# Kernel tuning notes

Measured on AMD Instinct MI355X. Metric: run time of the kernel, lower is better.

## Reference

```python
import jax, jax.numpy as jnp
import numpy as np

EMBED_DIM = 1024
N_HEADS = 16
HEAD_DIM = EMBED_DIM // N_HEADS  # 64
ROPE_DIM = 4
N_FREQ = HEAD_DIM // (2 * ROPE_DIM)  # 8 rotary freqs per coordinate axis
ROPE_THETA = 10000.0
FFN_DIM = 4 * EMBED_DIM
N_TOK = 4096
N_SEQ = 8
EPS = 1e-5
NEG_INF = -1e30


def setup_inputs() -> dict:
    key = jax.random.key(0)
    ks = jax.random.split(key, 16)
    s = 0.02
    coords = jax.random.uniform(ks[0], (N_TOK, ROPE_DIM), jnp.float32) * 10.0
    feats = jax.random.normal(ks[1], (N_TOK, EMBED_DIM), jnp.float32)
    interior = jnp.sort(jax.random.randint(ks[2], (N_SEQ - 1,), 1, N_TOK)).astype(jnp.int32)
    cu_seqlens = jnp.concatenate([jnp.zeros((1,), jnp.int32), interior,
                                  jnp.full((1,), N_TOK, jnp.int32)])
    # learnable RoPE inverse frequencies, one bank per coordinate axis
    base = 1.0 / (ROPE_THETA ** (jnp.arange(N_FREQ, dtype=jnp.float32) * 2.0 * ROPE_DIM / HEAD_DIM))
    inv_freq = jnp.tile(base[None, :], (ROPE_DIM, 1))  # [rope_dim, n_freq]
    return {
        "coords": coords,
        "feats": feats,
        "cu_seqlens": cu_seqlens,
        "Wqkv": jax.random.normal(ks[3], (EMBED_DIM, 3 * EMBED_DIM), jnp.float32) * s,
        "bqkv": jnp.zeros((3 * EMBED_DIM,), jnp.float32),
        "Wo": jax.random.normal(ks[4], (EMBED_DIM, EMBED_DIM), jnp.float32) * s,
        "bo": jnp.zeros((EMBED_DIM,), jnp.float32),
        "inv_freq": inv_freq,
        "ln1_g": jnp.ones((EMBED_DIM,), jnp.float32),
        "ln1_b": jnp.zeros((EMBED_DIM,), jnp.float32),
        "W1": jax.random.normal(ks[5], (EMBED_DIM, FFN_DIM), jnp.float32) * s,
        "b1": jnp.zeros((FFN_DIM,), jnp.float32),
        "W2": jax.random.normal(ks[6], (FFN_DIM, EMBED_DIM), jnp.float32) * s,
        "b2": jnp.zeros((EMBED_DIM,), jnp.float32),
        "ln2_g": jnp.ones((EMBED_DIM,), jnp.float32),
        "ln2_b": jnp.zeros((EMBED_DIM,), jnp.float32),
    }


def _layernorm(x, g, b):
    mu = jnp.mean(x, axis=-1, keepdims=True)
    xc = x - mu
    var = jnp.mean(xc * xc, axis=-1, keepdims=True)
    return xc * jax.lax.rsqrt(var + EPS) * g + b


def _block_forward(coords, feats, cu_seqlens, Wqkv, bqkv, Wo, bo, inv_freq,
                   ln1_g, ln1_b, W1, b1, W2, b2, ln2_g, ln2_b):
    N, D = feats.shape
    qkv = (feats @ Wqkv + bqkv).reshape(N, 3, N_HEADS, HEAD_DIM)
    q, k, v = qkv[:, 0], qkv[:, 1], qkv[:, 2]  # each [N, H, hd]

    # multi-dimensional learnable RoPE: each coord axis rotates its freq bank
    ang = jnp.einsum('nd,df->ndf', coords, inv_freq).reshape(N, 1, HEAD_DIM // 2)
    cos, sin = jnp.cos(ang), jnp.sin(ang)

    def rot(x):
        x1, x2 = jnp.split(x, 2, axis=-1)
        return jnp.concatenate([x1 * cos - x2 * sin, x2 * cos + x1 * sin], axis=-1)

    q, k = rot(q), rot(k)

    # varlen block-diagonal attention mask from cu_seqlens
    seg = jnp.searchsorted(cu_seqlens[1:], jnp.arange(N), side='right')
    mask = seg[:, None] == seg[None, :]  # [N, N]

    scores = jnp.einsum('nhd,mhd->hnm', q, k) / np.sqrt(HEAD_DIM).astype(np.float32)
    scores = jnp.where(mask[None, :, :], scores, NEG_INF)
    attn = jax.nn.softmax(scores, axis=-1)
    o = jnp.einsum('hnm,mhd->nhd', attn, v).reshape(N, D) @ Wo + bo

    h = _layernorm(feats + o, ln1_g, ln1_b)
    f = jax.nn.gelu(h @ W1 + b1) @ W2 + b2
    return _layernorm(h + f, ln2_g, ln2_b)


def reference(coords, feats, cu_seqlens, Wqkv, bqkv, Wo, bo, inv_freq,
              ln1_g, ln1_b, W1, b1, W2, b2, ln2_g, ln2_b):
    return _block_forward(coords, feats, cu_seqlens, Wqkv, bqkv, Wo, bo, inv_freq,
                          ln1_g, ln1_b, W1, b1, W2, b2, ln2_g, ln2_b)
```

## Files before the change

kernel.cpp:

```cpp
#include <hip/hip_runtime.h>

#define NTOK 4096
#define EMB  1024
#define NH   16
#define HD   64
#define FFN  4096

typedef __bf16 bf16x8 __attribute__((ext_vector_type(8)));
typedef float  f32x4  __attribute__((ext_vector_type(4)));

#define ASG __attribute__((address_space(1)))
#define ASL __attribute__((address_space(3)))

__device__ __forceinline__ float b2f(unsigned short u) {
    union { unsigned int i; float f; } v; v.i = ((unsigned int)u) << 16; return v.f;
}
__device__ __forceinline__ unsigned short f2b(float f) {
    return __builtin_bit_cast(unsigned short, (__bf16)f);
}
__device__ __forceinline__ float ldf(const void* p, size_t i, int f32) {
    return f32 ? ((const float*)p)[i] : b2f(((const unsigned short*)p)[i]);
}
__device__ __forceinline__ int probe_f32(const void* p) {
    return ((const unsigned int*)p)[0] == 0x3F800000u ? 1 : 0;
}
__device__ __forceinline__ float gelu_f(float x) {
    float z = 0.7978845608028654f * (x + 0.044715f * x * x * x);
    float t = 1.0f - 2.0f / (__expf(2.0f * z) + 1.0f);
    return 0.5f * x * (1.0f + t);
}
__device__ __forceinline__ void gll16(const void* g, void* l) {
    __builtin_amdgcn_global_load_lds((const ASG void*)g, (ASL void*)l, 16, 0, 0);
}

__global__ __launch_bounds__(256) void convert_kernel(
    const void* __restrict__ feats, const void* __restrict__ bqkv,
    const void* __restrict__ bo, const void* __restrict__ b1,
    const void* __restrict__ b2, const void* __restrict__ g1,
    const void* __restrict__ e1, const void* __restrict__ g2,
    const void* __restrict__ e2, const int* __restrict__ cu,
    unsigned short* __restrict__ feats_bf, unsigned short* __restrict__ smalls,
    int* __restrict__ seg, const void* __restrict__ pr) {
    const int f32 = probe_f32(pr);
    int bid = blockIdx.x, tid = threadIdx.x;
    if (bid < 4096) {
        size_t base = (size_t)bid * 1024 + tid * 4;
        union { unsigned short u[4]; int2 v; } U;
#pragma unroll
        for (int i = 0; i < 4; ++i) U.u[i] = f2b(ldf(feats, base + i, f32));
        *reinterpret_cast<int2*>(&feats_bf[base]) = U.v;
    } else if (bid < 4109) {
        int flat = (bid - 4096) * 1024 + tid * 4;
        const void* src; int off;
        if      (flat < 3072)  { src = bqkv; off = 0; }
        else if (flat < 4096)  { src = bo;   off = 3072; }
        else if (flat < 8192)  { src = b1;   off = 4096; }
        else if (flat < 9216)  { src = b2;   off = 8192; }
        else if (flat < 10240) { src = g1;   off = 9216; }
        else if (flat < 11264) { src = e1;   off = 10240; }
        else if (flat < 12288) { src = g2;   off = 11264; }
        else                   { src = e2;   off = 12288; }
        union { unsigned short u[4]; int2 v; } U;
#pragma unroll
        for (int i = 0; i < 4; ++i) U.u[i] = f2b(ldf(src, flat - off + i, f32));
        *reinterpret_cast<int2*>(&smalls[flat]) = U.v;
    } else {
        int n = (bid - 4109) * 256 + tid;
        int s = 0;
#pragma unroll
        for (int i = 1; i <= 8; ++i) s += (cu[i] <= n) ? 1 : 0;
        seg[n] = s;
    }
}

__global__ __launch_bounds__(64) void sched_kernel(
    const int* __restrict__ seg, const int* __restrict__ cu,
    int* __restrict__ perm) {
    __shared__ int w[64];
    int t = threadIdx.x;
    int s0 = seg[t * 64], s1 = seg[t * 64 + 63];
    int kb = cu[s0] & ~63;
    int kend = cu[s1 + 1];
    w[t] = (kend - kb + 63) >> 6;
    __syncthreads();
    int wt = w[t], r = 0;
#pragma unroll
    for (int j = 0; j < 64; ++j) {
        int wj = w[j];
        r += (wj > wt || (wj == wt && j < t)) ? 1 : 0;
    }
    perm[r] = t;
}

__global__ __launch_bounds__(256) void transpose_kernel(
    const void* __restrict__ W, unsigned short* __restrict__ O,
    int K, int N, const void* __restrict__ pr) {
    const int f32 = probe_f32(pr);
    int b = blockIdx.x, tid = threadIdx.x;
    int ntiles = N >> 6;
    int nt = b % ntiles, kt = b / ntiles;
    __shared__ unsigned short T[64][66];
    int cx = (tid & 15) * 4, ry = tid >> 4;
#pragma unroll
    for (int i = 0; i < 4; ++i) {
        int k = kt * 64 + ry + 16 * i;
        size_t base = (size_t)k * N + nt * 64 + cx;
#pragma unroll
        for (int j = 0; j < 4; ++j)
            T[ry + 16 * i][cx + j] = f2b(ldf(W, base + j, f32));
    }
    __syncthreads();
#pragma unroll
    for (int i = 0; i < 4; ++i) {
        int n = nt * 64 + ry + 16 * i;
        union { unsigned short u[4]; int2 v; } U;
#pragma unroll
        for (int j = 0; j < 4; ++j) U.u[j] = T[cx + j][ry + 16 * i];
        *reinterpret_cast<int2*>(&O[(size_t)n * K + kt * 64 + cx]) = U.v;
    }
}

template <int ACT, int OUTEXT, int TN, int SPLITV, int SPLITK>
__global__ __launch_bounds__(256) void gemm128(
    const unsigned short* __restrict__ A, const unsigned short* __restrict__ Bt,
    const unsigned short* __restrict__ bias, void* __restrict__ C,
    void* __restrict__ C2,
    int M, int N, int K, int lda, int ldb, const void* __restrict__ pr) {
    constexpr int NB = TN / 32;
    __shared__ __align__(16) unsigned short As[128 * 64];
    __shared__ __align__(16) unsigned short Bs[TN * 64];
    const int f32 = OUTEXT ? probe_f32(pr) : 0;
    const int tid = threadIdx.x;
    const int wave = tid >> 6, lane = tid & 63;
    const int wy = wave >> 1, wx = wave & 1;
    const int qm = lane & 15, quad = lane >> 4;
    const int z = SPLITK ? (int)blockIdx.z : 0;
    int bx, by;
    if ((gridDim.y & 7) == 0) {
        int lin = blockIdx.y * gridDim.x + blockIdx.x;
        int ypg = gridDim.y >> 3;
        int xcd = lin & 7, s = lin >> 3;
        int sy = s / gridDim.x;
        by = xcd * ypg + sy;
        bx = s - sy * gridDim.x;
    } else { bx = blockIdx.x; by = blockIdx.y; }
    const int m0 = by * 128, n0 = bx * TN;
    const int r = lane >> 3, gl = lane & 7;

    f32x4 acc[4][NB];
#pragma unroll
    for (int i = 0; i < 4; ++i)
#pragma unroll
        for (int j = 0; j < NB; ++j) acc[i][j] = (f32x4){0.f, 0.f, 0.f, 0.f};

    const int koff = SPLITK ? z * K : 0;
    const unsigned short* Ab = A  + (size_t)m0 * lda + koff;
    const unsigned short* Bb = Bt + (size_t)n0 * ldb + koff;

    for (int k0 = 0; k0 < K; k0 += 64) {
#pragma unroll
        for (int i = 0; i < 4; ++i) {
            int cc = wave * 4 + i;
            gll16(Ab + (size_t)(8 * cc + r) * lda + k0 + ((gl ^ r) << 3), &As[cc * 512]);
        }
#pragma unroll
        for (int i = 0; i < NB; ++i) {
            int cc = wave * NB + i;
            gll16(Bb + (size_t)(8 * cc + r) * ldb + k0 + ((gl ^ r) << 3), &Bs[cc * 512]);
        }
        __syncthreads();
#pragma unroll
        for (int h = 0; h < 2; ++h) {
            bf16x8 af[4], bfr[NB];
#pragma unroll
            for (int i = 0; i < 4; ++i) {
                int phys = (((h * 4 + quad) ^ (qm & 7)) << 3);
                af[i] = *reinterpret_cast<const bf16x8*>(&As[(64 * wy + 16 * i + qm) * 64 + phys]);
            }
#pragma unroll
            for (int j = 0; j < NB; ++j) {
                int phys = (((h * 4 + quad) ^ (qm & 7)) << 3);
                bfr[j] = *reinterpret_cast<const bf16x8*>(&Bs[((TN / 2) * wx + 16 * j + qm) * 64 + phys]);
            }
#pragma unroll
            for (int i = 0; i < 4; ++i)
#pragma unroll
                for (int j = 0; j < NB; ++j)
                    acc[i][j] = __builtin_amdgcn_mfma_f32_16x16x32_bf16(af[i], bfr[j], acc[i][j], 0, 0, 0);
        }
        __syncthreads();
    }
#pragma unroll
    for (int j = 0; j < NB; ++j) {
        int col = n0 + (TN / 2) * wx + 16 * j + qm;
        float bv = (SPLITK && z) ? 0.f : b2f(bias[col]);
        if (SPLITV && n0 >= 2048) {
            int d = col - 2048;
#pragma unroll
            for (int i = 0; i < 4; ++i) {
                int rowb = m0 + 64 * wy + 16 * i + quad * 4;
                union { unsigned short u[4]; int2 v; } U;
#pragma unroll
                for (int rr = 0; rr < 4; ++rr) U.u[rr] = f2b(acc[i][j][rr] + bv);
                *reinterpret_cast<int2*>((unsigned short*)C2 + (size_t)d * 4096 + rowb) = U.v;
            }
        } else {
            const int ldc = SPLITV ? 2048 : N;
            void* Cz = (SPLITK && z) ? C2 : C;
#pragma unroll
            for (int i = 0; i < 4; ++i) {
                int rowb = m0 + 64 * wy + 16 * i + quad * 4;
#pragma unroll
                for (int rr = 0; rr < 4; ++rr) {
                    size_t idx = (size_t)(rowb + rr) * ldc + col;
                    float v = acc[i][j][rr] + bv;
                    if (ACT == 1) v = gelu_f(v);
                    if (OUTEXT && f32) ((float*)Cz)[idx] = v;
                    else               ((unsigned short*)Cz)[idx] = f2b(v);
                }
            }
        }
    }
}

__global__ __launch_bounds__(512, 2) void gemm256_ffn1(
    const unsigned short* __restrict__ A, const unsigned short* __restrict__ Bt,
    const unsigned short* __restrict__ bias, unsigned short* __restrict__ C) {
    __shared__ __align__(16) unsigned short L[2][2][256][64];
    const int tid = threadIdx.x;
    const int wv = tid >> 6, lane = tid & 63;
    const int wm = wv >> 2, wn = wv & 3;
    const int qm = lane & 15, quad = lane >> 4;
    const int r8 = lane >> 3, gl = lane & 7;
    const int xsw = (gl ^ r8) << 3;
    int lin = blockIdx.y * 16 + blockIdx.x;
    int xcd = lin & 7, s = lin >> 3;
    int by = xcd * 2 + (s >> 4), bx = s & 15;
    const int m0 = by * 256, n0 = bx * 256;
    const unsigned short* Ab = A  + (size_t)m0 * 1024;
    const unsigned short* Bb = Bt + (size_t)n0 * 1024;

    f32x4 acc[8][4];
#pragma unroll
    for (int i = 0; i < 8; ++i)
#pragma unroll
        for (int j = 0; j < 4; ++j) acc[i][j] = (f32x4){0.f, 0.f, 0.f, 0.f};
    bf16x8 af[4], bf[4];

#define STG(buf, ten, sl, kn)                                                      \
    gll16(((ten) ? Bb : Ab) + (size_t)(64 * (sl) + 8 * wv + r8) * 1024 + (kn) + xsw, \
          &L[buf][ten][64 * (sl) + 8 * wv][0])
#define RD(mh, h)                                                                  \
    {                                                                              \
        const int phys = ((((h) * 4) + quad) ^ (qm & 7)) << 3;                     \
        _Pragma("unroll")                                                          \
        for (int i = 0; i < 4; ++i)                                                \
            af[i] = *reinterpret_cast<const bf16x8*>(                              \
                &Ac[(wm * 128 + (mh) * 64 + i * 16 + qm) * 64 + phys]);            \
        _Pragma("unroll")                                                          \
        for (int j = 0; j < 4; ++j)                                                \
            bf[j] = *reinterpret_cast<const bf16x8*>(                              \
                &Bc[(wn * 64 + j * 16 + qm) * 64 + phys]);                         \
    }
#define MM(mh, h)                                                                  \
    _Pragma("unroll")                                                              \
    for (int i = 0; i < 4; ++i)                                                    \
        _Pragma("unroll")                                                          \
        for (int j = 0; j < 4; ++j)                                                \
            acc[(mh) * 4 + i][j] = __builtin_amdgcn_mfma_f32_16x16x32_bf16(        \
                af[i], bf[j], acc[(mh) * 4 + i][j], 0, 0, 0);

    STG(0, 0, 0, 0); STG(0, 0, 2, 0);
    STG(0, 1, 0, 0); STG(0, 1, 1, 0); STG(0, 1, 2, 0); STG(0, 1, 3, 0);
    STG(0, 0, 1, 0); STG(0, 0, 3, 0);
    asm volatile("s_waitcnt vmcnt(2)" ::: "memory");
    __builtin_amdgcn_s_barrier();

    for (int t = 0; t < 16; ++t) {
        const unsigned short* Ac = &L[t & 1][0][0][0];
        const unsigned short* Bc = &L[t & 1][1][0][0];
        const int nb = (t + 1) & 1;
        const int kn = (t + 1) << 6;
        const bool more = t < 15;
        RD(0, 0);
        if (more) { STG(nb, 0, 0, kn); STG(nb, 0, 2, kn); }
        __builtin_amdgcn_s_barrier();
        asm volatile("s_waitcnt lgkmcnt(0)" ::: "memory");
        __builtin_amdgcn_s_setprio(1); MM(0, 0); __builtin_amdgcn_s_setprio(0);
        __builtin_amdgcn_s_barrier();
        RD(0, 1);
        if (more) {
            STG(nb, 1, 0, kn); STG(nb, 1, 1, kn);
            asm volatile("s_waitcnt vmcnt(4)" ::: "memory");
        } else {
            asm volatile("s_waitcnt vmcnt(0)" ::: "memory");
        }
        __builtin_amdgcn_s_barrier();
        asm volatile("s_waitcnt lgkmcnt(0)" ::: "memory");
        __builtin_amdgcn_s_setprio(1); MM(0, 1); __builtin_amdgcn_s_setprio(0);
        __builtin_amdgcn_s_barrier();
        RD(1, 0);
        if (more) { STG(nb, 1, 2, kn); STG(nb, 1, 3, kn); }
        __builtin_amdgcn_s_barrier();
        asm volatile("s_waitcnt lgkmcnt(0)" ::: "memory");
        __builtin_amdgcn_s_setprio(1); MM(1, 0); __builtin_amdgcn_s_setprio(0);
        __builtin_amdgcn_s_barrier();
        RD(1, 1);
        if (more) {
            STG(nb, 0, 1, kn); STG(nb, 0, 3, kn);
            asm volatile("s_waitcnt vmcnt(2)" ::: "memory");
        }
        __builtin_amdgcn_s_barrier();
        asm volatile("s_waitcnt lgkmcnt(0)" ::: "memory");
        __builtin_amdgcn_s_setprio(1); MM(1, 1); __builtin_amdgcn_s_setprio(0);
        __builtin_amdgcn_s_barrier();
    }
#undef STG
#undef RD
#undef MM
#pragma unroll
    for (int j = 0; j < 4; ++j) {
        int col = n0 + wn * 64 + j * 16 + qm;
        float bv = b2f(bias[col]);
#pragma unroll
        for (int i = 0; i < 8; ++i) {
            int rowb = m0 + wm * 128 + i * 16 + quad * 4;
#pragma unroll
            for (int rr = 0; rr < 4; ++rr) {
                float v = gelu_f(acc[i][j][rr] + bv);
                C[(size_t)(rowb + rr) * 4096 + col] = f2b(v);
            }
        }
    }
}

__global__ __launch_bounds__(256) void rope_kernel(
    const void* __restrict__ coords, const void* __restrict__ inv_freq,
    unsigned short* __restrict__ qk, const void* __restrict__ pr) {
    const int f32 = probe_f32(pr);
    int n = blockIdx.x, tid = threadIdx.x;
#pragma unroll
    for (int it = 0; it < 2; ++it) {
        int idx = tid + it * 256;
        int hh = idx >> 5, f = idx & 31;
        float c  = ldf(coords, n * 4 + (f >> 3), f32);
        float iv = ldf(inv_freq, f, f32);
        float sn, cs;
        sincosf(c * iv, &sn, &cs);
#pragma unroll
        for (int w = 0; w < 2; ++w) {
            size_t base = (size_t)n * 2048 + (size_t)w * 1024 + hh * 64;
            float scl = w ? 1.0f : 0.125f;
            float x1 = b2f(qk[base + f]);
            float x2 = b2f(qk[base + 32 + f]);
            qk[base + f]      = f2b((x1 * cs - x2 * sn) * scl);
            qk[base + 32 + f] = f2b((x2 * cs + x1 * sn) * scl);
        }
    }
}

__global__ __launch_bounds__(256) void attn_part(
    const unsigned short* __restrict__ qk, const unsigned short* __restrict__ vt,
    const int* __restrict__ seg, const int* __restrict__ cu,
    const int* __restrict__ perm,
    unsigned short* __restrict__ u0, unsigned short* __restrict__ u1,
    unsigned short* __restrict__ u2, float* __restrict__ ml) {
    const int h = blockIdx.x / 3;
    const int piece = blockIdx.x - 3 * h;
    const int t3 = perm[blockIdx.y];
    const int t0 = t3 * 64;
    const int tid  = threadIdx.x;
    const int wave = tid >> 6, lane = tid & 63;
    const int qm = lane & 15, quad = lane >> 4;

    __shared__ __align__(16) unsigned short Ks[2][64][64];
    __shared__ __align__(16) unsigned short Vs[2][80][64];
    __shared__ __align__(16) unsigned short Ps[64][64];
    __shared__ int segq[64], segk[2][64];

    const unsigned short* qrow = qk + (size_t)(t0 + 16 * wave + qm) * 2048 + h * 64;
    bf16x8 af0 = *reinterpret_cast<const bf16x8*>(qrow + quad * 8);
    bf16x8 af1 = *reinterpret_cast<const bf16x8*>(qrow + 32 + quad * 8);

    {
        int rr = tid >> 4, cc = (tid & 15) * 4;
        unsigned short val = (rr == 0) ? (unsigned short)0x3F80 : (unsigned short)0;
#pragma unroll
        for (int b = 0; b < 2; ++b)
#pragma unroll
            for (int j = 0; j < 4; ++j) Vs[b][64 + rr][cc + j] = val;
    }
    if (tid < 64) segq[tid] = seg[t0 + tid];
    __syncthreads();

    const int kbegA = cu[segq[0]] & ~63;
    const int kendT = cu[segq[63] + 1];
    const int nchunks = (kendT - kbegA + 63) >> 6;
    const int third = (nchunks + 2) / 3;
    const int kb = kbegA + piece * third * 64;
    const int ke = min(kendT, kbegA + (piece + 1) * third * 64);

    int sqr[4];
#pragma unroll
    for (int r = 0; r < 4; ++r) sqr[r] = segq[16 * wave + quad * 4 + r];
    const int wsmin = segq[16 * wave];
    const int wsmax = segq[16 * wave + 15];

    float m[4];
    f32x4 o[5];
#pragma unroll
    for (int r = 0; r < 4; ++r) m[r] = -1e30f;
#pragma unroll
    for (int t = 0; t < 5; ++t) o[t] = (f32x4){0.f, 0.f, 0.f, 0.f};

    const int krow = tid >> 2, kdc = (tid & 3) * 16;
    const int k7 = krow & 7;
    const int sw0 = (((tid & 3) * 2) ^ k7) << 3;
    const int sw1 = ((((tid & 3) * 2 + 1)) ^ k7) << 3;
    const int rsw0 = (quad ^ (qm & 7)) << 3;
    const int rsw1 = ((quad + 4) ^ (qm & 7)) << 3;
    int4 kA, kB, vA, vB; int sg;
#define LOAD_CHUNK(KC)                                                                   \
    {                                                                                    \
        const unsigned short* kp = qk + (size_t)((KC) + krow) * 2048 + 1024 + h * 64 + kdc; \
        kA = *reinterpret_cast<const int4*>(kp);                                         \
        kB = *reinterpret_cast<const int4*>(kp + 8);                                     \
        const unsigned short* vp = vt + (size_t)(h * 64 + krow) * 4096 + (KC) + kdc;     \
        vA = *reinterpret_cast<const int4*>(vp);                                         \
        vB = *reinterpret_cast<const int4*>(vp + 8);                                     \
        sg = 127;                                                                        \
        if (tid < 64 && (KC) + tid < ke) sg = seg[(KC) + tid];                           \
    }
#define STORE_CHUNK(B)                                                                   \
    {                                                                                    \
        *reinterpret_cast<int4*>(&Ks[B][krow][sw0]) = kA;                                \
        *reinterpret_cast<int4*>(&Ks[B][krow][sw1]) = kB;                                \
        *reinterpret_cast<int4*>(&Vs[B][krow][sw0]) = vA;                                \
        *reinterpret_cast<int4*>(&Vs[B][krow][sw1]) = vB;                                \
        if (tid < 64) segk[B][tid] = sg;                                                 \
    }

    int cur = 0;
    if (kb < ke) {
        LOAD_CHUNK(kb);
        STORE_CHUNK(0);
    }

    for (int kc = kb; kc < ke; kc += 64) {
        const bool have_next = (kc + 64 < ke);
        if (have_next) LOAD_CHUNK(kc + 64);
        __syncthreads();

        const int skmin = segk[cur][0], skmax = segk[cur][63];
        const bool act = !(skmax < wsmin || skmin > wsmax);

        if (act) {
            f32x4 sc[4];
#pragma unroll
            for (int nb = 0; nb < 4; ++nb) {
                bf16x8 bf0 = *reinterpret_cast<const bf16x8*>(&Ks[cur][16 * nb + qm][rsw0]);
                bf16x8 bf1 = *reinterpret_cast<const bf16x8*>(&Ks[cur][16 * nb + qm][rsw1]);
                f32x4 s = (f32x4){0.f, 0.f, 0.f, 0.f};
                s = __builtin_amdgcn_mfma_f32_16x16x32_bf16(af0, bf0, s, 0, 0, 0);
                s = __builtin_amdgcn_mfma_f32_16x16x32_bf16(af1, bf1, s, 0, 0, 0);
                sc[nb] = s;
            }
            if (!((skmin == skmax) & (wsmin == wsmax))) {
#pragma unroll
                for (int nb = 0; nb < 4; ++nb) {
                    int sk = segk[cur][16 * nb + qm];
#pragma unroll
                    for (int r = 0; r < 4; ++r)
                        sc[nb][r] = (sk == sqr[r]) ? sc[nb][r] : -1e30f;
                }
            }
            float alpha[4];
#pragma unroll
            for (int r = 0; r < 4; ++r) {
                float v = fmaxf(fmaxf(sc[0][r], sc[1][r]), fmaxf(sc[2][r], sc[3][r]));
                v = fmaxf(v, __shfl_xor(v, 1, 64));
                v = fmaxf(v, __shfl_xor(v, 2, 64));
                v = fmaxf(v, __shfl_xor(v, 4, 64));
                v = fmaxf(v, __shfl_xor(v, 8, 64));
                float mn = fmaxf(m[r], v);
                alpha[r] = __expf(m[r] - mn);
                m[r] = mn;
            }
#pragma unroll
            for (int nb = 0; nb < 4; ++nb) {
#pragma unroll
                for (int r = 0; r < 4; ++r) {
                    float p = __expf(sc[nb][r] - m[r]);
                    int row = 16 * wave + quad * 4 + r;
                    int phys = (((2 * nb + (qm >> 3)) ^ ((quad * 4 + r) & 7)) << 3) + (qm & 7);
                    Ps[row][phys] = f2b(p);
                }
            }
#pragma unroll
            for (int t = 0; t < 5; ++t)
#pragma unroll
                for (int r = 0; r < 4; ++r) o[t][r] *= alpha[r];

            bf16x8 pa0 = *reinterpret_cast<const bf16x8*>(&Ps[16 * wave + qm][rsw0]);
            bf16x8 pa1 = *reinterpret_cast<const bf16x8*>(&Ps[16 * wave + qm][rsw1]);
#pragma unroll
            for (int dt = 0; dt < 4; ++dt) {
                bf16x8 vb0 = *reinterpret_cast<const bf16x8*>(&Vs[cur][16 * dt + qm][rsw0]);
                bf16x8 vb1 = *reinterpret_cast<const bf16x8*>(&Vs[cur][16 * dt + qm][rsw1]);
                o[dt] = __builtin_amdgcn_mfma_f32_16x16x32_bf16(pa0, vb0, o[dt], 0, 0, 0);
                o[dt] = __builtin_amdgcn_mfma_f32_16x16x32_bf16(pa1, vb1, o[dt], 0, 0, 0);
            }
            {
                bf16x8 vb0 = *reinterpret_cast<const bf16x8*>(&Vs[cur][64 + qm][rsw0]);
                bf16x8 vb1 = *reinterpret_cast<const bf16x8*>(&Vs[cur][64 + qm][rsw1]);
                o[4] = __builtin_amdgcn_mfma_f32_16x16x32_bf16(pa0, vb0, o[4], 0, 0, 0);
                o[4] = __builtin_amdgcn_mfma_f32_16x16x32_bf16(pa1, vb1, o[4], 0, 0, 0);
            }
        }
        if (have_next) {
            STORE_CHUNK(cur ^ 1);
        }
        cur ^= 1;
    }
#undef LOAD_CHUNK
#undef STORE_CHUNK
    unsigned short* dst = (piece == 0) ? u0 : ((piece == 1) ? u1 : u2);
#pragma unroll
    for (int dt = 0; dt < 4; ++dt)
#pragma unroll
        for (int r = 0; r < 4; ++r) {
            int row = t0 + 16 * wave + quad * 4 + r;
            dst[(size_t)row * 1024 + h * 64 + 16 * dt + qm] = f2b(o[dt][r]);
        }
    if (qm == 0) {
        float2* ML = (float2*)ml;
#pragma unroll
        for (int r = 0; r < 4; ++r) {
            int row = t0 + 16 * wave + quad * 4 + r;
            ML[((piece * 16 + h) << 12) + row] = make_float2(m[r], o[4][r]);
        }
    }
}

__global__ __launch_bounds__(256) void combine_kernel(
    const unsigned short* __restrict__ u1, const unsigned short* __restrict__ u2,
    const float* __restrict__ ml, unsigned short* __restrict__ u0out) {
    int n = blockIdx.x, tid = threadIdx.x;
    int d4 = tid * 4, h = tid >> 4;
    const float2* ML = (const float2*)ml;
    float2 p0 = ML[(h << 12) + n];
    float2 p1 = ML[((16 + h) << 12) + n];
    float2 p2 = ML[((32 + h) << 12) + n];
    float M = fmaxf(p0.x, fmaxf(p1.x, p2.x));
    float a0 = __expf(p0.x - M), a1 = __expf(p1.x - M), a2 = __expf(p2.x - M);
    float rcp = 1.0f / (a0 * p0.y + a1 * p1.y + a2 * p2.y);
    size_t ix = (size_t)n * 1024 + d4;
    union { int2 q; unsigned short u[4]; } A, B, Cq, R;
    A.q  = *reinterpret_cast<const int2*>(u0out + ix);
    B.q  = *reinterpret_cast<const int2*>(u1 + ix);
    Cq.q = *reinterpret_cast<const int2*>(u2 + ix);
#pragma unroll
    for (int i = 0; i < 4; ++i)
        R.u[i] = f2b((a0 * b2f(A.u[i]) + a1 * b2f(B.u[i]) + a2 * b2f(Cq.u[i])) * rcp);
    *reinterpret_cast<int2*>(u0out + ix) = R.q;
}

template <int OUTEXT>
__global__ __launch_bounds__(256) void ln3_kernel(
    const unsigned short* __restrict__ x1, const unsigned short* __restrict__ x2a,
    const unsigned short* __restrict__ x2b,
    const unsigned short* __restrict__ g, const unsigned short* __restrict__ b,
    void* __restrict__ out, const void* __restrict__ pr) {
    const int f32 = probe_f32(pr);
    int n = blockIdx.x, tid = threadIdx.x;
    __shared__ float red[8];
    const int d0 = tid * 4;
    const size_t ix0 = (size_t)n * EMB + d0;
    float v[4];
    {
        union { int2 q; unsigned short u[4]; } A, Ba, Bb2;
        A.q   = *reinterpret_cast<const int2*>(&x1[ix0]);
        Ba.q  = *reinterpret_cast<const int2*>(&x2a[ix0]);
        Bb2.q = *reinterpret_cast<const int2*>(&x2b[ix0]);
#pragma unroll
        for (int i = 0; i < 4; ++i)
            v[i] = b2f(A.u[i]) + b2f(Ba.u[i]) + b2f(Bb2.u[i]);
    }
    float s = v[0] + v[1] + v[2] + v[3];
#pragma unroll
    for (int off = 1; off < 64; off <<= 1) s += __shfl_xor(s, off, 64);
    if ((tid & 63) == 0) red[tid >> 6] = s;
    __syncthreads();
    float mu = (red[0] + red[1] + red[2] + red[3]) * (1.0f / 1024.0f);
    float sq = 0.0f;
#pragma unroll
    for (int i = 0; i < 4; ++i) { float c = v[i] - mu; sq += c * c; }
#pragma unroll
    for (int off = 1; off < 64; off <<= 1) sq += __shfl_xor(sq, off, 64);
    if ((tid & 63) == 0) red[4 + (tid >> 6)] = sq;
    __syncthreads();
    float var = (red[4] + red[5] + red[6] + red[7]) * (1.0f / 1024.0f);
    float rcp = rsqrtf(var + 1e-5f);
    union { int2 q; unsigned short u[4]; } G, Bb;
    G.q  = *reinterpret_cast<const int2*>(&g[d0]);
    Bb.q = *reinterpret_cast<const int2*>(&b[d0]);
    if (OUTEXT && f32) {
        float4 R;
        R.x = (v[0] - mu) * rcp * b2f(G.u[0]) + b2f(Bb.u[0]);
        R.y = (v[1] - mu) * rcp * b2f(G.u[1]) + b2f(Bb.u[1]);
        R.z = (v[2] - mu) * rcp * b2f(G.u[2]) + b2f(Bb.u[2]);
        R.w = (v[3] - mu) * rcp * b2f(G.u[3]) + b2f(Bb.u[3]);
        *reinterpret_cast<float4*>((float*)out + ix0) = R;
    } else {
        union { int2 q; unsigned short u[4]; } R;
#pragma unroll
        for (int i = 0; i < 4; ++i)
            R.u[i] = f2b((v[i] - mu) * rcp * b2f(G.u[i]) + b2f(Bb.u[i]));
        *reinterpret_cast<int2*>((unsigned short*)out + ix0) = R.q;
    }
}

extern "C" void kernel_launch(void* const* d_in, const int* in_sizes, int n_in,
                              void* d_out, int out_size, void* d_ws, size_t ws_size,
                              hipStream_t stream) {
    const void* coords   = d_in[0];
    const void* feats    = d_in[1];
    const int*  cu       = (const int*)d_in[2];
    const void* Wqkv     = d_in[3];
    const void* bqkv     = d_in[4];
    const void* Wo       = d_in[5];
    const void* bo       = d_in[6];
    const void* inv_freq = d_in[7];
    const void* ln1_g    = d_in[8];
    const void* ln1_b    = d_in[9];
    const void* W1       = d_in[10];
    const void* b1       = d_in[11];
    const void* W2       = d_in[12];
    const void* b2       = d_in[13];
    const void* ln2_g    = d_in[14];
    const void* ln2_b    = d_in[15];
    const void* pr = ln1_g;

    char* ws = (char*)d_ws;
    int* seg = (int*)ws;
    unsigned short* smalls   = (unsigned short*)(ws + 16384);
    unsigned short* bqkv_bf  = smalls;
    unsigned short* bo_bf    = smalls + 3072;
    unsigned short* b1_bf    = smalls + 4096;
    unsigned short* b2_bf    = smalls + 8192;
    unsigned short* g1_bf    = smalls + 9216;
    unsigned short* e1_bf    = smalls + 10240;
    unsigned short* g2_bf    = smalls + 11264;
    unsigned short* e2_bf    = smalls + 12288;
    int* perm                = (int*)(ws + 49152);
    unsigned short* feats_bf = (unsigned short*)(ws + 65536);
    unsigned short* hbuf     = feats_bf;
    unsigned short* W1_t     = (unsigned short*)(ws + 8454144);
    unsigned short* u1buf    = (unsigned short*)(ws + 16842752);
    unsigned short* Wqkv_t   = (unsigned short*)(ws + 18939904);
    unsigned short* qkbuf    = (unsigned short*)(ws + 25231360);
    unsigned short* vtbuf    = (unsigned short*)(ws + 42008576);
    unsigned short* attn_o   = (unsigned short*)(ws + 50397184);
    unsigned short* Wo_t     = (unsigned short*)(ws + 18939904);
    unsigned short* woP0     = (unsigned short*)(ws + 25231360);
    unsigned short* woP1     = (unsigned short*)(ws + 33619968);
    unsigned short* f1       = (unsigned short*)(ws + 25231360);
    unsigned short* ffP0     = (unsigned short*)(ws + 8454144);
    unsigned short* ffP1     = (unsigned short*)(ws + 16842752);
    float* mlbuf = (float*)d_out;
    unsigned short* u2buf = (unsigned short*)((char*)d_out + 2097152);
    unsigned short* W2_t  = (unsigned short*)((char*)d_out + 8388608);

    hipLaunchKernelGGL(convert_kernel, dim3(4125), dim3(256), 0, stream,
                       feats, bqkv, bo, b1, b2, ln1_g, ln1_b, ln2_g, ln2_b, cu,
                       feats_bf, smalls, seg, pr);
    hipLaunchKernelGGL(sched_kernel, dim3(1), dim3(64), 0, stream,
                       seg, cu, perm);
    hipLaunchKernelGGL(transpose_kernel, dim3(768), dim3(256), 0, stream,
                       Wqkv, Wqkv_t, 1024, 3072, pr);
    hipLaunchKernelGGL(transpose_kernel, dim3(1024), dim3(256), 0, stream,
                       W1, W1_t, 1024, 4096, pr);
    hipLaunchKernelGGL((gemm128<0, 0, 128, 1, 0>), dim3(24, 32), dim3(256), 0, stream,
                       feats_bf, Wqkv_t, bqkv_bf, qkbuf, vtbuf, NTOK, 3072, 1024, 1024, 1024, pr);
    hipLaunchKernelGGL(rope_kernel, dim3(NTOK), dim3(256), 0, stream,
                       coords, inv_freq, qkbuf, pr);
    hipLaunchKernelGGL(attn_part, dim3(48, 64), dim3(256), 0, stream,
                       qkbuf, vtbuf, seg, cu, perm, attn_o, u1buf, u2buf, mlbuf);
    hipLaunchKernelGGL(combine_kernel, dim3(NTOK), dim3(256), 0, stream,
                       u1buf, u2buf, mlbuf, attn_o);
    hipLaunchKernelGGL(transpose_kernel, dim3(256), dim3(256), 0, stream,
                       Wo, Wo_t, 1024, 1024, pr);
    hipLaunchKernelGGL((gemm128<0, 0, 128, 0, 1>), dim3(8, 32, 2), dim3(256), 0, stream,
                       attn_o, Wo_t, bo_bf, woP0, woP1, NTOK, 1024, 512, 1024, 1024, pr);
    hipLaunchKernelGGL(transpose_kernel, dim3(1024), dim3(256), 0, stream,
                       W2, W2_t, 4096, 1024, pr);
    hipLaunchKernelGGL((ln3_kernel<0>), dim3(NTOK), dim3(256), 0, stream,
                       feats_bf, woP0, woP1, g1_bf, e1_bf, hbuf, pr);
    hipLaunchKernelGGL(gemm256_ffn1, dim3(16, 16), dim3(512), 0, stream,
                       hbuf, W1_t, b1_bf, f1);
    hipLaunchKernelGGL((gemm128<0, 0, 128, 0, 1>), dim3(8, 32, 2), dim3(256), 0, stream,
                       f1, W2_t, b2_bf, ffP0, ffP1, NTOK, 1024, 2048, 4096, 4096, pr);
    hipLaunchKernelGGL((ln3_kernel<1>), dim3(NTOK), dim3(256), 0, stream,
                       hbuf, ffP0, ffP1, g2_bf, e2_bf, d_out, pr);
}
```

Before: 378.3 us.

## Fuse prep, schedule and weight transposes into one kernel; fold RoPE into QKV GEMM

Merges the conversion, scheduling and three weight-transpose launches into a single prep kernel, which cuts launch count and lets independent small jobs share one grid. RoPE rotation and Q scaling move into the QKV GEMM epilogue, so qkbuf is no longer written, reread and rewritten by a separate pass. Wo_t is moved into a buffer in d_out so it does not clash with qkbuf. The epilogue writes scalar bf16 values per lane with strided addresses and recomputes sincos for every element, so store efficiency may be lower than the old packed path.

```diff
diff --git a/kernel.cpp b/kernel.cpp
--- a/kernel.cpp
+++ b/kernel.cpp
@@ -33,14 +33,45 @@
     __builtin_amdgcn_global_load_lds((const ASG void*)g, (ASL void*)l, 16, 0, 0);
 }
 
-__global__ __launch_bounds__(256) void convert_kernel(
+__device__ __forceinline__ void transpose_body(
+    const void* __restrict__ W, unsigned short* __restrict__ O,
+    int K, int N, int b, int f32, unsigned short (*T)[66], int tid) {
+    int ntiles = N >> 6;
+    int nt = b % ntiles, kt = b / ntiles;
+    int cx = (tid & 15) * 4, ry = tid >> 4;
+#pragma unroll
+    for (int i = 0; i < 4; ++i) {
+        int k = kt * 64 + ry + 16 * i;
+        size_t base = (size_t)k * N + nt * 64 + cx;
+#pragma unroll
+        for (int j = 0; j < 4; ++j)
+            T[ry + 16 * i][cx + j] = f2b(ldf(W, base + j, f32));
+    }
+    __syncthreads();
+#pragma unroll
+    for (int i = 0; i < 4; ++i) {
+        int n = nt * 64 + ry + 16 * i;
+        union { unsigned short u[4]; int2 v; } U;
+#pragma unroll
+        for (int j = 0; j < 4; ++j) U.u[j] = T[cx + j][ry + 16 * i];
+        *reinterpret_cast<int2*>(&O[(size_t)n * K + kt * 64 + cx]) = U.v;
+    }
+}
+
+__global__ __launch_bounds__(256) void prep_kernel(
     const void* __restrict__ feats, const void* __restrict__ bqkv,
     const void* __restrict__ bo, const void* __restrict__ b1,
     const void* __restrict__ b2, const void* __restrict__ g1,
     const void* __restrict__ e1, const void* __restrict__ g2,
     const void* __restrict__ e2, const int* __restrict__ cu,
+    const void* __restrict__ Wqkv, const void* __restrict__ W1,
+    const void* __restrict__ Wo,
     unsigned short* __restrict__ feats_bf, unsigned short* __restrict__ smalls,
-    int* __restrict__ seg, const void* __restrict__ pr) {
+    int* __restrict__ seg, int* __restrict__ perm,
+    unsigned short* __restrict__ Wqkv_t, unsigned short* __restrict__ W1_t,
+    unsigned short* __restrict__ Wo_t, const void* __restrict__ pr) {
+    __shared__ unsigned short T[64][66];
+    __shared__ int w[64];
     const int f32 = probe_f32(pr);
     int bid = blockIdx.x, tid = threadIdx.x;
     if (bid < 4096) {
@@ -64,72 +95,63 @@
 #pragma unroll
         for (int i = 0; i < 4; ++i) U.u[i] = f2b(ldf(src, flat - off + i, f32));
         *reinterpret_cast<int2*>(&smalls[flat]) = U.v;
-    } else {
+    } else if (bid < 4125) {
         int n = (bid - 4109) * 256 + tid;
         int s = 0;
 #pragma unroll
         for (int i = 1; i <= 8; ++i) s += (cu[i] <= n) ? 1 : 0;
         seg[n] = s;
-    }
-}
-
-__global__ __launch_bounds__(64) void sched_kernel(
-    const int* __restrict__ seg, const int* __restrict__ cu,
-    int* __restrict__ perm) {
-    __shared__ int w[64];
-    int t = threadIdx.x;
-    int s0 = seg[t * 64], s1 = seg[t * 64 + 63];
-    int kb = cu[s0] & ~63;
-    int kend = cu[s1 + 1];
-    w[t] = (kend - kb + 63) >> 6;
-    __syncthreads();
-    int wt = w[t], r = 0;
-#pragma unroll
-    for (int j = 0; j < 64; ++j) {
-        int wj = w[j];
-        r += (wj > wt || (wj == wt && j < t)) ? 1 : 0;
-    }
-    perm[r] = t;
+    } else if (bid == 4125) {
+        if (tid < 64) {
+            int n0s = tid * 64, n1s = tid * 64 + 63;
+            int s0 = 0, s1 = 0;
+#pragma unroll
+            for (int i = 1; i <= 8; ++i) {
+                s0 += (cu[i] <= n0s) ? 1 : 0;
+                s1 += (cu[i] <= n1s) ? 1 : 0;
+            }
+            int kb = cu[s0] & ~63;
+            int kend = cu[s1 + 1];
+            w[tid] = (kend - kb + 63) >> 6;
+        }
+        __syncthreads();
+        if (tid < 64) {
+            int wt = w[tid], r = 0;
+#pragma unroll
+            for (int j = 0; j < 64; ++j) {
+                int wj = w[j];
+                r += (wj > wt || (wj == wt && j < tid)) ? 1 : 0;
+            }
+            perm[r] = tid;
+        }
+    } else if (bid < 4894) {
+        transpose_body(Wqkv, Wqkv_t, 1024, 3072, bid - 4126, f32, T, tid);
+    } else if (bid < 5918) {
+        transpose_body(W1, W1_t, 1024, 4096, bid - 4894, f32, T, tid);
+    } else {
+        transpose_body(Wo, Wo_t, 1024, 1024, bid - 5918, f32, T, tid);
+    }
 }
 
 __global__ __launch_bounds__(256) void transpose_kernel(
     const void* __restrict__ W, unsigned short* __restrict__ O,
     int K, int N, const void* __restrict__ pr) {
+    __shared__ unsigned short T[64][66];
     const int f32 = probe_f32(pr);
-    int b = blockIdx.x, tid = threadIdx.x;
-    int ntiles = N >> 6;
-    int nt = b % ntiles, kt = b / ntiles;
-    __shared__ unsigned short T[64][66];
-    int cx = (tid & 15) * 4, ry = tid >> 4;
-#pragma unroll
-    for (int i = 0; i < 4; ++i) {
-        int k = kt * 64 + ry + 16 * i;
-        size_t base = (size_t)k * N + nt * 64 + cx;
-#pragma unroll
-        for (int j = 0; j < 4; ++j)
-            T[ry + 16 * i][cx + j] = f2b(ldf(W, base + j, f32));
-    }
-    __syncthreads();
-#pragma unroll
-    for (int i = 0; i < 4; ++i) {
-        int n = nt * 64 + ry + 16 * i;
-        union { unsigned short u[4]; int2 v; } U;
-#pragma unroll
-        for (int j = 0; j < 4; ++j) U.u[j] = T[cx + j][ry + 16 * i];
-        *reinterpret_cast<int2*>(&O[(size_t)n * K + kt * 64 + cx]) = U.v;
-    }
-}
-
-template <int ACT, int OUTEXT, int TN, int SPLITV, int SPLITK>
+    transpose_body(W, O, K, N, blockIdx.x, f32, T, threadIdx.x);
+}
+
+template <int ACT, int OUTEXT, int TN, int SPLITV, int SPLITK, int ROPE>
 __global__ __launch_bounds__(256) void gemm128(
     const unsigned short* __restrict__ A, const unsigned short* __restrict__ Bt,
     const unsigned short* __restrict__ bias, void* __restrict__ C,
     void* __restrict__ C2,
-    int M, int N, int K, int lda, int ldb, const void* __restrict__ pr) {
+    int M, int N, int K, int lda, int ldb, const void* __restrict__ pr,
+    const void* __restrict__ coords, const void* __restrict__ inv_freq) {
     constexpr int NB = TN / 32;
     __shared__ __align__(16) unsigned short As[128 * 64];
     __shared__ __align__(16) unsigned short Bs[TN * 64];
-    const int f32 = OUTEXT ? probe_f32(pr) : 0;
+    const int f32 = (OUTEXT || ROPE) ? probe_f32(pr) : 0;
     const int tid = threadIdx.x;
     const int wave = tid >> 6, lane = tid & 63;
     const int wy = wave >> 1, wx = wave & 1;
@@ -189,6 +211,34 @@
                     acc[i][j] = __builtin_amdgcn_mfma_f32_16x16x32_bf16(af[i], bfr[j], acc[i][j], 0, 0, 0);
         }
         __syncthreads();
+    }
+    if (ROPE && n0 < 2048) {
+#pragma unroll
+        for (int jp = 0; jp < 2; ++jp) {
+            int colA = n0 + 64 * wx + 16 * jp + qm;
+            int colB = colA + 32;
+            int f = colA & 31;
+            float iv  = ldf(inv_freq, f, f32);
+            float bvA = b2f(bias[colA]);
+            float bvB = b2f(bias[colB]);
+            float scl = (colA < 1024) ? 0.125f : 1.0f;
+#pragma unroll
+            for (int i = 0; i < 4; ++i) {
+                int rowb = m0 + 64 * wy + 16 * i + quad * 4;
+#pragma unroll
+                for (int rr = 0; rr < 4; ++rr) {
+                    int row = rowb + rr;
+                    float c = ldf(coords, (size_t)row * 4 + (f >> 3), f32);
+                    float sn, cs;
+                    sincosf(c * iv, &sn, &cs);
+                    float x1 = acc[i][jp][rr] + bvA;
+                    float x2 = acc[i][jp + 2][rr] + bvB;
+                    ((unsigned short*)C)[(size_t)row * 2048 + colA] = f2b((x1 * cs - x2 * sn) * scl);
+                    ((unsigned short*)C)[(size_t)row * 2048 + colB] = f2b((x2 * cs + x1 * sn) * scl);
+                }
+            }
+        }
+        return;
     }
 #pragma unroll
     for (int j = 0; j < NB; ++j) {
@@ -330,31 +380,6 @@
                 float v = gelu_f(acc[i][j][rr] + bv);
                 C[(size_t)(rowb + rr) * 4096 + col] = f2b(v);
             }
-        }
-    }
-}
-
-__global__ __launch_bounds__(256) void rope_kernel(
-    const void* __restrict__ coords, const void* __restrict__ inv_freq,
-    unsigned short* __restrict__ qk, const void* __restrict__ pr) {
-    const int f32 = probe_f32(pr);
-    int n = blockIdx.x, tid = threadIdx.x;
-#pragma unroll
-    for (int it = 0; it < 2; ++it) {
-        int idx = tid + it * 256;
-        int hh = idx >> 5, f = idx & 31;
-        float c  = ldf(coords, n * 4 + (f >> 3), f32);
-        float iv = ldf(inv_freq, f, f32);
-        float sn, cs;
-        sincosf(c * iv, &sn, &cs);
-#pragma unroll
-        for (int w = 0; w < 2; ++w) {
-            size_t base = (size_t)n * 2048 + (size_t)w * 1024 + hh * 64;
-            float scl = w ? 1.0f : 0.125f;
-            float x1 = b2f(qk[base + f]);
-            float x2 = b2f(qk[base + 32 + f]);
-            qk[base + f]      = f2b((x1 * cs - x2 * sn) * scl);
-            qk[base + 32 + f] = f2b((x2 * cs + x1 * sn) * scl);
         }
     }
 }
@@ -661,7 +686,6 @@
     unsigned short* qkbuf    = (unsigned short*)(ws + 25231360);
     unsigned short* vtbuf    = (unsigned short*)(ws + 42008576);
     unsigned short* attn_o   = (unsigned short*)(ws + 50397184);
-    unsigned short* Wo_t     = (unsigned short*)(ws + 18939904);
     unsigned short* woP0     = (unsigned short*)(ws + 25231360);
     unsigned short* woP1     = (unsigned short*)(ws + 33619968);
     unsigned short* f1       = (unsigned short*)(ws + 25231360);
@@ -670,36 +694,31 @@
     float* mlbuf = (float*)d_out;
     unsigned short* u2buf = (unsigned short*)((char*)d_out + 2097152);
     unsigned short* W2_t  = (unsigned short*)((char*)d_out + 8388608);
-
-    hipLaunchKernelGGL(convert_kernel, dim3(4125), dim3(256), 0, stream,
+    unsigned short* Wo_t  = (unsigned short*)((char*)d_out + 11534336);
+
+    hipLaunchKernelGGL(prep_kernel, dim3(6174), dim3(256), 0, stream,
                        feats, bqkv, bo, b1, b2, ln1_g, ln1_b, ln2_g, ln2_b, cu,
-                       feats_bf, smalls, seg, pr);
-    hipLaunchKernelGGL(sched_kernel, dim3(1), dim3(64), 0, stream,
-                       seg, cu, perm);
-    hipLaunchKernelGGL(transpose_kernel, dim3(768), dim3(256), 0, stream,
-                       Wqkv, Wqkv_t, 1024, 3072, pr);
-    hipLaunchKernelGGL(transpose_kernel, dim3(1024), dim3(256), 0, stream,
-                       W1, W1_t, 1024, 4096, pr);
-    hipLaunchKernelGGL((gemm128<0, 0, 128, 1, 0>), dim3(24, 32), dim3(256), 0, stream,
-                       feats_bf, Wqkv_t, bqkv_bf, qkbuf, vtbuf, NTOK, 3072, 1024, 1024, 1024, pr);
-    hipLaunchKernelGGL(rope_kernel, dim3(NTOK), dim3(256), 0, stream,
-                       coords, inv_freq, qkbuf, pr);
+                       Wqkv, W1, Wo,
+                       feats_bf, smalls, seg, perm, Wqkv_t, W1_t, Wo_t, pr);
+    hipLaunchKernelGGL((gemm128<0, 0, 128, 1, 0, 1>), dim3(24, 32), dim3(256), 0, stream,
+                       feats_bf, Wqkv_t, bqkv_bf, qkbuf, vtbuf, NTOK, 3072, 1024, 1024, 1024, pr,
+                       coords, inv_freq);
     hipLaunchKernelGGL(attn_part, dim3(48, 64), dim3(256), 0, stream,
                        qkbuf, vtbuf, seg, cu, perm, attn_o, u1buf, u2buf, mlbuf);
     hipLaunchKernelGGL(combine_kernel, dim3(NTOK), dim3(256), 0, stream,
                        u1buf, u2buf, mlbuf, attn_o);
-    hipLaunchKernelGGL(transpose_kernel, dim3(256), dim3(256), 0, stream,
-                       Wo, Wo_t, 1024, 1024, pr);
-    hipLaunchKernelGGL((gemm128<0, 0, 128, 0, 1>), dim3(8, 32, 2), dim3(256), 0, stream,
-                       attn_o, Wo_t, bo_bf, woP0, woP1, NTOK, 1024, 512, 1024, 1024, pr);
+    hipLaunchKernelGGL((gemm128<0, 0, 128, 0, 1, 0>), dim3(8, 32, 2), dim3(256), 0, stream,
+                       attn_o, Wo_t, bo_bf, woP0, woP1, NTOK, 1024, 512, 1024, 1024, pr,
+                       nullptr, nullptr);
     hipLaunchKernelGGL(transpose_kernel, dim3(1024), dim3(256), 0, stream,
                        W2, W2_t, 4096, 1024, pr);
     hipLaunchKernelGGL((ln3_kernel<0>), dim3(NTOK), dim3(256), 0, stream,
                        feats_bf, woP0, woP1, g1_bf, e1_bf, hbuf, pr);
     hipLaunchKernelGGL(gemm256_ffn1, dim3(16, 16), dim3(512), 0, stream,
                        hbuf, W1_t, b1_bf, f1);
-    hipLaunchKernelGGL((gemm128<0, 0, 128, 0, 1>), dim3(8, 32, 2), dim3(256), 0, stream,
-                       f1, W2_t, b2_bf, ffP0, ffP1, NTOK, 1024, 2048, 4096, 4096, pr);
+    hipLaunchKernelGGL((gemm128<0, 0, 128, 0, 1, 0>), dim3(8, 32, 2), dim3(256), 0, stream,
+                       f1, W2_t, b2_bf, ffP0, ffP1, NTOK, 1024, 2048, 4096, 4096, pr,
+                       nullptr, nullptr);
     hipLaunchKernelGGL((ln3_kernel<1>), dim3(NTOK), dim3(256), 0, stream,
                        hbuf, ffP0, ffP1, g2_bf, e2_bf, d_out, pr);
 }
```

Result: slower. 406.1 us (+7.3%).
